# Kernel tuning notes

Measured on AMD Instinct MI355X. Metric: run time of the kernel, lower is better.

Reference implementation:

```python
import jax, jax.numpy as jnp
import numpy as np
import math

B, S, H, K = 512, 200, 256, 16

def setup_inputs() -> dict:
    key = jax.random.key(0)
    ks = jax.random.split(key, 8)
    scale = 1.0 / math.sqrt(H)
    return {
        "input_tensor": jax.random.normal(ks[0], (B, S, H), dtype=jnp.float32),
        "item_mask": jax.random.randint(ks[1], (B, S, 1), 0, 2) > 0,
        "time_f_w_matrix": jax.random.uniform(ks[2], (B, S, 1), dtype=jnp.float32),
        "W1": jax.random.normal(ks[3], (H, H), dtype=jnp.float32) * scale,
        "b1": jnp.zeros((H,), dtype=jnp.float32),
        "W2": jax.random.normal(ks[4], (H, H), dtype=jnp.float32) * scale,
        "b2": jnp.zeros((H,), dtype=jnp.float32),
        "W3": jax.random.normal(ks[5], (H, K), dtype=jnp.float32) * scale,
    }

def reference(input_tensor, item_mask, time_f_w_matrix, W1, b1, W2, b2, W3):
    # small MLP: two Linear+ReLU then bias-free Linear to k_interests
    h = jax.nn.relu(jnp.einsum('bsh,hd->bsd', input_tensor, W1) + b1)
    h = jax.nn.relu(jnp.einsum('bsh,hd->bsd', h, W2) + b2)
    D = jnp.einsum('bsh,hk->bsk', h, W3)              # [B,S,K]
    D = jax.nn.softmax(D, axis=-1)                    # softmax over interests
    mask = item_mask[:, :, 0:1]                       # [B,S,1] bool, broadcast over K
    D = jnp.where(mask, D, jnp.float32(-10000.0))
    D = D / jnp.float32(math.sqrt(K))
    D = jax.nn.softmax(D, axis=-2)                    # softmax over sequence
    D = time_f_w_matrix[:, :, 0:1] * D                # time weighting
    # einsum 'nij,nik->nkj': pool items into K interest vectors
    return jnp.einsum('bsh,bsk->bkh', input_tensor, D)
```

## Files before the change

kernel.cpp:

```cpp
#include <hip/hip_runtime.h>
#include <math.h>

#define HDIM 256
#define KDIM 16
#define SDIM 200
#define BDIM 512
#define NROWS (BDIM * SDIM)
#define TM 32

typedef __bf16 bf16x8 __attribute__((ext_vector_type(8)));
typedef __bf16 bf16x4 __attribute__((ext_vector_type(4)));
typedef float  f32x4  __attribute__((ext_vector_type(4)));

__global__ __launch_bounds__(256) void pack_w_kernel(
    const float* __restrict__ src, __bf16* __restrict__ hi,
    __bf16* __restrict__ lo, int lgN)
{
    int idx = blockIdx.x * 256 + threadIdx.x;
    int N = 1 << lgN;
    int k = idx >> lgN;
    int n = idx & (N - 1);
    float v = src[idx];
    __bf16 h = (__bf16)v;
    float r = v - (float)h;
    int d = (((k >> 3) << lgN) + n) * 8 + (k & 7);
    hi[d] = h;
    lo[d] = (__bf16)r;
}

__global__ __launch_bounds__(256, 4) void mlp_softk_mfma(
    const float* __restrict__ X, const int* __restrict__ mask,
    const __bf16* __restrict__ W1h, const __bf16* __restrict__ W1l,
    const float* __restrict__ b1,
    const __bf16* __restrict__ W2h, const __bf16* __restrict__ W2l,
    const float* __restrict__ b2,
    const __bf16* __restrict__ W3h, const __bf16* __restrict__ W3l,
    float* __restrict__ P)
{
    __shared__ __bf16 Ahi[TM * HDIM];
    __shared__ __bf16 Alo[TM * HDIM];

    const int tid  = threadIdx.x;
    const int lane = tid & 63;
    const int w    = tid >> 6;
    const int l15  = lane & 15;
    const int quad = lane >> 4;
    const long r0  = (long)blockIdx.x * TM;

    {
        const float4* Xt = (const float4*)(X + r0 * HDIM);
        #pragma unroll
        for (int t = 0; t < (TM * HDIM / 4) / 256; ++t) {
            int v4  = tid + t * 256;
            float4 f = Xt[v4];
            int row = v4 >> 6;
            int col = (v4 & 63) << 2;
            int kgs = (col >> 3) ^ (row & 31);
            int base = row * HDIM + kgs * 8 + (col & 7);
            __bf16 h0 = (__bf16)f.x, h1 = (__bf16)f.y,
                   h2 = (__bf16)f.z, h3 = (__bf16)f.w;
            bf16x4 hv = {h0, h1, h2, h3};
            bf16x4 lv = {(__bf16)(f.x - (float)h0), (__bf16)(f.y - (float)h1),
                         (__bf16)(f.z - (float)h2), (__bf16)(f.w - (float)h3)};
            *(bf16x4*)(&Ahi[base]) = hv;
            *(bf16x4*)(&Alo[base]) = lv;
        }
    }
    __syncthreads();

    f32x4 acc[2][4];

    auto layer = [&](const __bf16* __restrict__ Wh, const __bf16* __restrict__ Wl,
                     const float* __restrict__ bias) {
        #pragma unroll
        for (int mt = 0; mt < 2; ++mt)
            #pragma unroll
            for (int nt = 0; nt < 4; ++nt)
                acc[mt][nt] = (f32x4){0.f, 0.f, 0.f, 0.f};

        #pragma unroll 2
        for (int kc = 0; kc < 8; ++kc) {
            bf16x8 bh[4], bl[4], ah[2], al[2];
            #pragma unroll
            for (int nt = 0; nt < 4; ++nt) {
                int n  = w * 64 + nt * 16 + l15;
                int kg = kc * 4 + quad;
                bh[nt] = *(const bf16x8*)(Wh + (kg * HDIM + n) * 8);
                bl[nt] = *(const bf16x8*)(Wl + (kg * HDIM + n) * 8);
            }
            #pragma unroll
            for (int mt = 0; mt < 2; ++mt) {
                int row = mt * 16 + l15;
                int kgs = (kc * 4 + quad) ^ (row & 31);
                ah[mt] = *(const bf16x8*)(&Ahi[row * HDIM + kgs * 8]);
                al[mt] = *(const bf16x8*)(&Alo[row * HDIM + kgs * 8]);
            }
            #pragma unroll
            for (int mt = 0; mt < 2; ++mt)
                #pragma unroll
                for (int nt = 0; nt < 4; ++nt) {
                    acc[mt][nt] = __builtin_amdgcn_mfma_f32_16x16x32_bf16(
                        ah[mt], bh[nt], acc[mt][nt], 0, 0, 0);
                    acc[mt][nt] = __builtin_amdgcn_mfma_f32_16x16x32_bf16(
                        al[mt], bh[nt], acc[mt][nt], 0, 0, 0);
                    acc[mt][nt] = __builtin_amdgcn_mfma_f32_16x16x32_bf16(
                        ah[mt], bl[nt], acc[mt][nt], 0, 0, 0);
                }
        }
        __syncthreads();

        float bias_v[4];
        #pragma unroll
        for (int nt = 0; nt < 4; ++nt) bias_v[nt] = bias[w * 64 + nt * 16 + l15];
        #pragma unroll
        for (int mt = 0; mt < 2; ++mt)
            #pragma unroll
            for (int nt = 0; nt < 4; ++nt)
                #pragma unroll
                for (int r = 0; r < 4; ++r) {
                    float v = fmaxf(acc[mt][nt][r] + bias_v[nt], 0.f);
                    int row = mt * 16 + quad * 4 + r;
                    int col = w * 64 + nt * 16 + l15;
                    int idx = row * HDIM + (((col >> 3) ^ (row & 31)) * 8) + (col & 7);
                    __bf16 h = (__bf16)v;
                    Ahi[idx] = h;
                    Alo[idx] = (__bf16)(v - (float)h);
                }
        __syncthreads();
    };

    layer(W1h, W1l, b1);
    layer(W2h, W2l, b2);

    if (w < 2) {
        f32x4 lg = {0.f, 0.f, 0.f, 0.f};
        #pragma unroll
        for (int kc = 0; kc < 8; ++kc) {
            int row = w * 16 + l15;
            int kg  = kc * 4 + quad;
            int kgs = kg ^ (row & 31);
            bf16x8 ah = *(const bf16x8*)(&Ahi[row * HDIM + kgs * 8]);
            bf16x8 al = *(const bf16x8*)(&Alo[row * HDIM + kgs * 8]);
            bf16x8 bh = *(const bf16x8*)(W3h + (kg * KDIM + l15) * 8);
            bf16x8 bl = *(const bf16x8*)(W3l + (kg * KDIM + l15) * 8);
            lg = __builtin_amdgcn_mfma_f32_16x16x32_bf16(ah, bh, lg, 0, 0, 0);
            lg = __builtin_amdgcn_mfma_f32_16x16x32_bf16(al, bh, lg, 0, 0, 0);
            lg = __builtin_amdgcn_mfma_f32_16x16x32_bf16(ah, bl, lg, 0, 0, 0);
        }

        #pragma unroll
        for (int r = 0; r < 4; ++r) {
            float v  = lg[r];
            float mx = v;
            mx = fmaxf(mx, __shfl_xor(mx, 1));
            mx = fmaxf(mx, __shfl_xor(mx, 2));
            mx = fmaxf(mx, __shfl_xor(mx, 4));
            mx = fmaxf(mx, __shfl_xor(mx, 8));
            float e = __expf(v - mx);
            float s = e;
            s += __shfl_xor(s, 1);
            s += __shfl_xor(s, 2);
            s += __shfl_xor(s, 4);
            s += __shfl_xor(s, 8);
            int grow = (int)r0 + w * 16 + quad * 4 + r;
            int mv   = mask[grow];
            float ov = mv ? (e / s) * 0.25f : -2500.0f;
            P[(long)grow * KDIM + l15] = ov;
        }
    }
}

__global__ __launch_bounds__(256) void softs_agg_kernel(
    const float* __restrict__ X, const float* __restrict__ tf,
    const float* __restrict__ P, float* __restrict__ out)
{
    __shared__ float wl[SDIM * KDIM];
    __shared__ float tfl[SDIM];
    __shared__ float psum[256];
    __shared__ float invk[KDIM];
    __shared__ float red[KDIM * HDIM];

    const int tid = threadIdx.x;
    const int b   = blockIdx.x;

    const float* Pb = P + (long)b * SDIM * KDIM;
    float ps = 0.f;
    #pragma unroll
    for (int t = 0; t < 13; ++t) {
        int i = tid + t * 256;
        if (i < SDIM * KDIM) {
            float e = __expf(Pb[i]);
            wl[i] = e;
            ps += e;
        }
    }
    psum[tid] = ps;
    if (tid < SDIM) tfl[tid] = tf[b * SDIM + tid];
    __syncthreads();

    if (tid < KDIM) {
        float s = 0.f;
        #pragma unroll
        for (int g = 0; g < 16; ++g) s += psum[tid + g * 16];
        invk[tid] = 1.f / s;
    }
    __syncthreads();

    #pragma unroll
    for (int t = 0; t < 13; ++t) {
        int i = tid + t * 256;
        if (i < SDIM * KDIM) wl[i] *= tfl[i >> 4] * invk[i & 15];
    }
    __syncthreads();

    const int wv = tid >> 6;
    const int sh = wv >> 1;
    const int hh = wv & 1;
    const int ln = tid & 63;

    float accx[KDIM], accy[KDIM];
    #pragma unroll
    for (int k = 0; k < KDIM; ++k) { accx[k] = 0.f; accy[k] = 0.f; }

    const float2* Xb  = (const float2*)(X + (long)b * SDIM * HDIM) + hh * 64 + ln;
    const f32x4*  wl4 = (const f32x4*)wl;
    const int s0 = sh * 100;
    #pragma unroll 4
    for (int si = 0; si < 100; ++si) {
        int s = s0 + si;
        float2 x = Xb[(long)s * (HDIM / 2)];
        f32x4 d0 = wl4[s * 4 + 0];
        f32x4 d1 = wl4[s * 4 + 1];
        f32x4 d2 = wl4[s * 4 + 2];
        f32x4 d3 = wl4[s * 4 + 3];
        #pragma unroll
        for (int j = 0; j < 4; ++j) {
            accx[0 + j]  = fmaf(x.x, d0[j], accx[0 + j]);
            accx[4 + j]  = fmaf(x.x, d1[j], accx[4 + j]);
            accx[8 + j]  = fmaf(x.x, d2[j], accx[8 + j]);
            accx[12 + j] = fmaf(x.x, d3[j], accx[12 + j]);
            accy[0 + j]  = fmaf(x.y, d0[j], accy[0 + j]);
            accy[4 + j]  = fmaf(x.y, d1[j], accy[4 + j]);
            accy[8 + j]  = fmaf(x.y, d2[j], accy[8 + j]);
            accy[12 + j] = fmaf(x.y, d3[j], accy[12 + j]);
        }
    }

    if (sh == 1) {
        #pragma unroll
        for (int k = 0; k < KDIM; ++k) {
            red[k * HDIM + hh * 128 + 2 * ln + 0] = accx[k];
            red[k * HDIM + hh * 128 + 2 * ln + 1] = accy[k];
        }
    }
    __syncthreads();
    if (sh == 0) {
        float* ob = out + (long)b * KDIM * HDIM + hh * 128 + 2 * ln;
        #pragma unroll
        for (int k = 0; k < KDIM; ++k) {
            float2 o;
            o.x = accx[k] + red[k * HDIM + hh * 128 + 2 * ln + 0];
            o.y = accy[k] + red[k * HDIM + hh * 128 + 2 * ln + 1];
            *(float2*)(ob + (long)k * HDIM) = o;
        }
    }
}

extern "C" void kernel_launch(void* const* d_in, const int* in_sizes, int n_in,
                              void* d_out, int out_size, void* d_ws, size_t ws_size,
                              hipStream_t stream) {
    (void)in_sizes; (void)n_in; (void)out_size; (void)ws_size;
    const float* X    = (const float*)d_in[0];
    const int*   mask = (const int*)  d_in[1];
    const float* tf   = (const float*)d_in[2];
    const float* W1   = (const float*)d_in[3];
    const float* b1   = (const float*)d_in[4];
    const float* W2   = (const float*)d_in[5];
    const float* b2   = (const float*)d_in[6];
    const float* W3   = (const float*)d_in[7];
    float* out = (float*)d_out;

    char* ws = (char*)d_ws;
    float*  P   = (float*)ws;
    __bf16* w1h = (__bf16*)(ws + 6553600);
    __bf16* w1l = w1h + 65536;
    __bf16* w2h = w1l + 65536;
    __bf16* w2l = w2h + 65536;
    __bf16* w3h = w2l + 65536;
    __bf16* w3l = w3h + 4096;

    pack_w_kernel<<<256, 256, 0, stream>>>(W1, w1h, w1l, 8);
    pack_w_kernel<<<256, 256, 0, stream>>>(W2, w2h, w2l, 8);
    pack_w_kernel<<<16,  256, 0, stream>>>(W3, w3h, w3l, 4);
    mlp_softk_mfma<<<NROWS / TM, 256, 0, stream>>>(X, mask, w1h, w1l, b1,
                                                   w2h, w2l, b2, w3h, w3l, P);
    softs_agg_kernel<<<BDIM, 256, 0, stream>>>(X, tf, P, out);
}
```

Measured before the change: 285.2 us.

## Register-resident single-wave MLP with transposed MFMA and bias folded into weights

Rewrites the MLP kernel so each 64-thread wave handles 32 rows entirely in registers. It computes W^T·X^T so layer outputs stay in MFMA accumulators and are passed to the next layer through lane shuffles instead of shared memory and __syncthreads. Biases are folded in as an extra K chunk multiplied by a ones vector. The three weight-pack launches are merged into one kernel with the new fragment layout. This removes LDS traffic and block barriers, but raises register pressure heavily (a 16x2 accumulator array plus 8x2 fragment arrays per wave) and has each wave reload all weights from cache.

After: 325.5 us. +14.1%, slower.

```diff
diff --git a/kernel.cpp b/kernel.cpp
--- a/kernel.cpp
+++ b/kernel.cpp
@@ -6,167 +6,225 @@
 #define SDIM 200
 #define BDIM 512
 #define NROWS (BDIM * SDIM)
-#define TM 32
 
 typedef __bf16 bf16x8 __attribute__((ext_vector_type(8)));
-typedef __bf16 bf16x4 __attribute__((ext_vector_type(4)));
 typedef float  f32x4  __attribute__((ext_vector_type(4)));
 
-__global__ __launch_bounds__(256) void pack_w_kernel(
-    const float* __restrict__ src, __bf16* __restrict__ hi,
-    __bf16* __restrict__ lo, int lgN)
+#define MFMA(a, b, c) __builtin_amdgcn_mfma_f32_16x16x32_bf16(a, b, c, 0, 0, 0)
+
+__global__ __launch_bounds__(256) void pack_all(
+    const float* __restrict__ W1, const float* __restrict__ b1,
+    const float* __restrict__ W2, const float* __restrict__ b2,
+    const float* __restrict__ W3,
+    __bf16* __restrict__ w1h, __bf16* __restrict__ w1l,
+    __bf16* __restrict__ w2h, __bf16* __restrict__ w2l,
+    __bf16* __restrict__ w3h, __bf16* __restrict__ w3l)
 {
-    int idx = blockIdx.x * 256 + threadIdx.x;
-    int N = 1 << lgN;
-    int k = idx >> lgN;
-    int n = idx & (N - 1);
-    float v = src[idx];
+    int gid = blockIdx.x * 256 + threadIdx.x;
+    const float *src, *bias;
+    __bf16 *oh, *ol;
+    int e, N;
+    if (gid < 73728)       { src = W1; bias = b1;      oh = w1h; ol = w1l; e = gid;          N = 256; }
+    else if (gid < 147456) { src = W2; bias = b2;      oh = w2h; ol = w2l; e = gid - 73728;  N = 256; }
+    else if (gid < 151552) { src = W3; bias = nullptr; oh = w3h; ol = w3l; e = gid - 147456; N = 16;  }
+    else return;
+
+    int j = e & 7, l = (e >> 3) & 63, c = e >> 9;
+    int dt, kc;
+    if (N == 256) { dt = c & 15; kc = c >> 4; } else { dt = 0; kc = c; }
+    int d = dt * 16 + (l & 15);
+    int k = kc * 32 + ((l >> 4) * 8) + j;
+    float v = (k < 256) ? src[k * N + d] : ((k == 256 && bias) ? bias[d] : 0.f);
     __bf16 h = (__bf16)v;
-    float r = v - (float)h;
-    int d = (((k >> 3) << lgN) + n) * 8 + (k & 7);
-    hi[d] = h;
-    lo[d] = (__bf16)r;
+    oh[e] = h;
+    ol[e] = (__bf16)(v - (float)h);
 }
 
-__global__ __launch_bounds__(256, 4) void mlp_softk_mfma(
+__global__ __launch_bounds__(64, 2) void mlp_fused(
     const float* __restrict__ X, const int* __restrict__ mask,
-    const __bf16* __restrict__ W1h, const __bf16* __restrict__ W1l,
-    const float* __restrict__ b1,
-    const __bf16* __restrict__ W2h, const __bf16* __restrict__ W2l,
-    const float* __restrict__ b2,
-    const __bf16* __restrict__ W3h, const __bf16* __restrict__ W3l,
+    const __bf16* __restrict__ w1h, const __bf16* __restrict__ w1l,
+    const __bf16* __restrict__ w2h, const __bf16* __restrict__ w2l,
+    const __bf16* __restrict__ w3h, const __bf16* __restrict__ w3l,
     float* __restrict__ P)
 {
-    __shared__ __bf16 Ahi[TM * HDIM];
-    __shared__ __bf16 Alo[TM * HDIM];
-
-    const int tid  = threadIdx.x;
-    const int lane = tid & 63;
-    const int w    = tid >> 6;
-    const int l15  = lane & 15;
-    const int quad = lane >> 4;
-    const long r0  = (long)blockIdx.x * TM;
-
+    const int l = threadIdx.x;
+    const int q = l >> 4, m = l & 15;
+    const long R = (long)blockIdx.x * 32;
+
+    f32x4 acc1[16][2];
+    #pragma unroll
+    for (int t = 0; t < 16; ++t) {
+        acc1[t][0] = (f32x4){0.f, 0.f, 0.f, 0.f};
+        acc1[t][1] = (f32x4){0.f, 0.f, 0.f, 0.f};
+    }
+
+    #pragma unroll 1
+    for (int kc = 0; kc < 8; ++kc) {
+        bf16x8 bxh[2], bxl[2];
+        #pragma unroll
+        for (int rt = 0; rt < 2; ++rt) {
+            const float* xp = X + (R + rt * 16 + m) * HDIM + kc * 32 + q * 8;
+            float4 f0 = *(const float4*)xp;
+            float4 f1 = *(const float4*)(xp + 4);
+            float xv[8] = {f0.x, f0.y, f0.z, f0.w, f1.x, f1.y, f1.z, f1.w};
+            #pragma unroll
+            for (int j2 = 0; j2 < 8; ++j2) {
+                __bf16 h = (__bf16)xv[j2];
+                bxh[rt][j2] = h;
+                bxl[rt][j2] = (__bf16)(xv[j2] - (float)h);
+            }
+        }
+        #pragma unroll
+        for (int dt = 0; dt < 16; ++dt) {
+            bf16x8 ah = *(const bf16x8*)(w1h + (kc * 16 + dt) * 512 + l * 8);
+            bf16x8 al = *(const bf16x8*)(w1l + (kc * 16 + dt) * 512 + l * 8);
+            #pragma unroll
+            for (int rt = 0; rt < 2; ++rt) {
+                acc1[dt][rt] = MFMA(ah, bxh[rt], acc1[dt][rt]);
+                acc1[dt][rt] = MFMA(al, bxh[rt], acc1[dt][rt]);
+                acc1[dt][rt] = MFMA(ah, bxl[rt], acc1[dt][rt]);
+            }
+        }
+    }
     {
-        const float4* Xt = (const float4*)(X + r0 * HDIM);
-        #pragma unroll
-        for (int t = 0; t < (TM * HDIM / 4) / 256; ++t) {
-            int v4  = tid + t * 256;
-            float4 f = Xt[v4];
-            int row = v4 >> 6;
-            int col = (v4 & 63) << 2;
-            int kgs = (col >> 3) ^ (row & 31);
-            int base = row * HDIM + kgs * 8 + (col & 7);
-            __bf16 h0 = (__bf16)f.x, h1 = (__bf16)f.y,
-                   h2 = (__bf16)f.z, h3 = (__bf16)f.w;
-            bf16x4 hv = {h0, h1, h2, h3};
-            bf16x4 lv = {(__bf16)(f.x - (float)h0), (__bf16)(f.y - (float)h1),
-                         (__bf16)(f.z - (float)h2), (__bf16)(f.w - (float)h3)};
-            *(bf16x4*)(&Ahi[base]) = hv;
-            *(bf16x4*)(&Alo[base]) = lv;
-        }
-    }
-    __syncthreads();
-
-    f32x4 acc[2][4];
-
-    auto layer = [&](const __bf16* __restrict__ Wh, const __bf16* __restrict__ Wl,
-                     const float* __restrict__ bias) {
-        #pragma unroll
-        for (int mt = 0; mt < 2; ++mt)
-            #pragma unroll
-            for (int nt = 0; nt < 4; ++nt)
-                acc[mt][nt] = (f32x4){0.f, 0.f, 0.f, 0.f};
-
-        #pragma unroll 2
-        for (int kc = 0; kc < 8; ++kc) {
-            bf16x8 bh[4], bl[4], ah[2], al[2];
-            #pragma unroll
-            for (int nt = 0; nt < 4; ++nt) {
-                int n  = w * 64 + nt * 16 + l15;
-                int kg = kc * 4 + quad;
-                bh[nt] = *(const bf16x8*)(Wh + (kg * HDIM + n) * 8);
-                bl[nt] = *(const bf16x8*)(Wl + (kg * HDIM + n) * 8);
-            }
-            #pragma unroll
-            for (int mt = 0; mt < 2; ++mt) {
-                int row = mt * 16 + l15;
-                int kgs = (kc * 4 + quad) ^ (row & 31);
-                ah[mt] = *(const bf16x8*)(&Ahi[row * HDIM + kgs * 8]);
-                al[mt] = *(const bf16x8*)(&Alo[row * HDIM + kgs * 8]);
-            }
-            #pragma unroll
-            for (int mt = 0; mt < 2; ++mt)
+        bf16x8 bx1;
+        #pragma unroll
+        for (int j2 = 0; j2 < 8; ++j2) bx1[j2] = (__bf16)0.f;
+        bx1[0] = (q == 0) ? (__bf16)1.f : (__bf16)0.f;
+        #pragma unroll
+        for (int dt = 0; dt < 16; ++dt) {
+            bf16x8 ah = *(const bf16x8*)(w1h + (128 + dt) * 512 + l * 8);
+            bf16x8 al = *(const bf16x8*)(w1l + (128 + dt) * 512 + l * 8);
+            #pragma unroll
+            for (int rt = 0; rt < 2; ++rt) {
+                acc1[dt][rt] = MFMA(ah, bx1, acc1[dt][rt]);
+                acc1[dt][rt] = MFMA(al, bx1, acc1[dt][rt]);
+            }
+        }
+    }
+
+    bf16x8 f2h[8][2], f2l[8][2];
+    #pragma unroll
+    for (int kc2 = 0; kc2 < 8; ++kc2) {
+        #pragma unroll
+        for (int rt = 0; rt < 2; ++rt) {
+            float g[8];
+            #pragma unroll
+            for (int i = 0; i < 4; ++i) {
+                float s0 = fmaxf(acc1[2 * kc2 + 0][rt][i], 0.f);
+                float s1 = fmaxf(acc1[2 * kc2 + 1][rt][i], 0.f);
+                int lane_lo = ((2 * (q & 1)) << 4) | m;
+                float glo0 = __shfl(s0, lane_lo);
+                float ghi0 = __shfl(s0, lane_lo + 16);
+                float glo1 = __shfl(s1, lane_lo);
+                float ghi1 = __shfl(s1, lane_lo + 16);
+                g[i]     = (q < 2) ? glo0 : glo1;
+                g[4 + i] = (q < 2) ? ghi0 : ghi1;
+            }
+            #pragma unroll
+            for (int j2 = 0; j2 < 8; ++j2) {
+                __bf16 h = (__bf16)g[j2];
+                f2h[kc2][rt][j2] = h;
+                f2l[kc2][rt][j2] = (__bf16)(g[j2] - (float)h);
+            }
+        }
+    }
+
+    f32x4 acc3[2] = {(f32x4){0.f, 0.f, 0.f, 0.f}, (f32x4){0.f, 0.f, 0.f, 0.f}};
+    #pragma unroll 1
+    for (int qd = 0; qd < 4; ++qd) {
+        f32x4 acc2[4][2];
+        #pragma unroll
+        for (int t = 0; t < 4; ++t) {
+            acc2[t][0] = (f32x4){0.f, 0.f, 0.f, 0.f};
+            acc2[t][1] = (f32x4){0.f, 0.f, 0.f, 0.f};
+        }
+        #pragma unroll
+        for (int kc2 = 0; kc2 < 8; ++kc2) {
+            #pragma unroll
+            for (int dtl = 0; dtl < 4; ++dtl) {
+                int c = kc2 * 16 + qd * 4 + dtl;
+                bf16x8 ah = *(const bf16x8*)(w2h + c * 512 + l * 8);
+                bf16x8 al = *(const bf16x8*)(w2l + c * 512 + l * 8);
                 #pragma unroll
-                for (int nt = 0; nt < 4; ++nt) {
-                    acc[mt][nt] = __builtin_amdgcn_mfma_f32_16x16x32_bf16(
-                        ah[mt], bh[nt], acc[mt][nt], 0, 0, 0);
-                    acc[mt][nt] = __builtin_amdgcn_mfma_f32_16x16x32_bf16(
-                        al[mt], bh[nt], acc[mt][nt], 0, 0, 0);
-                    acc[mt][nt] = __builtin_amdgcn_mfma_f32_16x16x32_bf16(
-                        ah[mt], bl[nt], acc[mt][nt], 0, 0, 0);
+                for (int rt = 0; rt < 2; ++rt) {
+                    acc2[dtl][rt] = MFMA(ah, f2h[kc2][rt], acc2[dtl][rt]);
+                    acc2[dtl][rt] = MFMA(al, f2h[kc2][rt], acc2[dtl][rt]);
+                    acc2[dtl][rt] = MFMA(ah, f2l[kc2][rt], acc2[dtl][rt]);
                 }
-        }
-        __syncthreads();
-
-        float bias_v[4];
-        #pragma unroll
-        for (int nt = 0; nt < 4; ++nt) bias_v[nt] = bias[w * 64 + nt * 16 + l15];
-        #pragma unroll
-        for (int mt = 0; mt < 2; ++mt)
-            #pragma unroll
-            for (int nt = 0; nt < 4; ++nt)
+            }
+        }
+        {
+            bf16x8 bx1;
+            #pragma unroll
+            for (int j2 = 0; j2 < 8; ++j2) bx1[j2] = (__bf16)0.f;
+            bx1[0] = (q == 0) ? (__bf16)1.f : (__bf16)0.f;
+            #pragma unroll
+            for (int dtl = 0; dtl < 4; ++dtl) {
+                int c = 128 + qd * 4 + dtl;
+                bf16x8 ah = *(const bf16x8*)(w2h + c * 512 + l * 8);
+                bf16x8 al = *(const bf16x8*)(w2l + c * 512 + l * 8);
                 #pragma unroll
-                for (int r = 0; r < 4; ++r) {
-                    float v = fmaxf(acc[mt][nt][r] + bias_v[nt], 0.f);
-                    int row = mt * 16 + quad * 4 + r;
-                    int col = w * 64 + nt * 16 + l15;
-                    int idx = row * HDIM + (((col >> 3) ^ (row & 31)) * 8) + (col & 7);
-                    __bf16 h = (__bf16)v;
-                    Ahi[idx] = h;
-                    Alo[idx] = (__bf16)(v - (float)h);
+                for (int rt = 0; rt < 2; ++rt) {
+                    acc2[dtl][rt] = MFMA(ah, bx1, acc2[dtl][rt]);
+                    acc2[dtl][rt] = MFMA(al, bx1, acc2[dtl][rt]);
                 }
-        __syncthreads();
-    };
-
-    layer(W1h, W1l, b1);
-    layer(W2h, W2l, b2);
-
-    if (w < 2) {
-        f32x4 lg = {0.f, 0.f, 0.f, 0.f};
-        #pragma unroll
-        for (int kc = 0; kc < 8; ++kc) {
-            int row = w * 16 + l15;
-            int kg  = kc * 4 + quad;
-            int kgs = kg ^ (row & 31);
-            bf16x8 ah = *(const bf16x8*)(&Ahi[row * HDIM + kgs * 8]);
-            bf16x8 al = *(const bf16x8*)(&Alo[row * HDIM + kgs * 8]);
-            bf16x8 bh = *(const bf16x8*)(W3h + (kg * KDIM + l15) * 8);
-            bf16x8 bl = *(const bf16x8*)(W3l + (kg * KDIM + l15) * 8);
-            lg = __builtin_amdgcn_mfma_f32_16x16x32_bf16(ah, bh, lg, 0, 0, 0);
-            lg = __builtin_amdgcn_mfma_f32_16x16x32_bf16(al, bh, lg, 0, 0, 0);
-            lg = __builtin_amdgcn_mfma_f32_16x16x32_bf16(ah, bl, lg, 0, 0, 0);
-        }
-
-        #pragma unroll
-        for (int r = 0; r < 4; ++r) {
-            float v  = lg[r];
-            float mx = v;
-            mx = fmaxf(mx, __shfl_xor(mx, 1));
-            mx = fmaxf(mx, __shfl_xor(mx, 2));
-            mx = fmaxf(mx, __shfl_xor(mx, 4));
-            mx = fmaxf(mx, __shfl_xor(mx, 8));
-            float e = __expf(v - mx);
-            float s = e;
-            s += __shfl_xor(s, 1);
-            s += __shfl_xor(s, 2);
-            s += __shfl_xor(s, 4);
-            s += __shfl_xor(s, 8);
-            int grow = (int)r0 + w * 16 + quad * 4 + r;
-            int mv   = mask[grow];
-            float ov = mv ? (e / s) * 0.25f : -2500.0f;
-            P[(long)grow * KDIM + l15] = ov;
-        }
+            }
+        }
+        #pragma unroll
+        for (int c = 0; c < 2; ++c) {
+            bf16x8 f3h[2], f3l[2];
+            #pragma unroll
+            for (int rt = 0; rt < 2; ++rt) {
+                float g[8];
+                #pragma unroll
+                for (int i = 0; i < 4; ++i) {
+                    float s0 = fmaxf(acc2[2 * c + 0][rt][i], 0.f);
+                    float s1 = fmaxf(acc2[2 * c + 1][rt][i], 0.f);
+                    int lane_lo = ((2 * (q & 1)) << 4) | m;
+                    float glo0 = __shfl(s0, lane_lo);
+                    float ghi0 = __shfl(s0, lane_lo + 16);
+                    float glo1 = __shfl(s1, lane_lo);
+                    float ghi1 = __shfl(s1, lane_lo + 16);
+                    g[i]     = (q < 2) ? glo0 : glo1;
+                    g[4 + i] = (q < 2) ? ghi0 : ghi1;
+                }
+                #pragma unroll
+                for (int j2 = 0; j2 < 8; ++j2) {
+                    __bf16 h = (__bf16)g[j2];
+                    f3h[rt][j2] = h;
+                    f3l[rt][j2] = (__bf16)(g[j2] - (float)h);
+                }
+            }
+            bf16x8 a3h = *(const bf16x8*)(w3h + (2 * qd + c) * 512 + l * 8);
+            bf16x8 a3l = *(const bf16x8*)(w3l + (2 * qd + c) * 512 + l * 8);
+            #pragma unroll
+            for (int rt = 0; rt < 2; ++rt) {
+                acc3[rt] = MFMA(a3h, f3h[rt], acc3[rt]);
+                acc3[rt] = MFMA(a3l, f3h[rt], acc3[rt]);
+                acc3[rt] = MFMA(a3h, f3l[rt], acc3[rt]);
+            }
+        }
+    }
+
+    #pragma unroll
+    for (int rt = 0; rt < 2; ++rt) {
+        float mx = fmaxf(fmaxf(acc3[rt][0], acc3[rt][1]),
+                         fmaxf(acc3[rt][2], acc3[rt][3]));
+        mx = fmaxf(mx, __shfl_xor(mx, 16));
+        mx = fmaxf(mx, __shfl_xor(mx, 32));
+        float e[4], s = 0.f;
+        #pragma unroll
+        for (int r = 0; r < 4; ++r) { e[r] = __expf(acc3[rt][r] - mx); s += e[r]; }
+        s += __shfl_xor(s, 16);
+        s += __shfl_xor(s, 32);
+        long grow = R + rt * 16 + m;
+        int mv = mask[grow];
+        float inv = 0.25f / s;
+        float4 o;
+        if (mv) { o.x = e[0] * inv; o.y = e[1] * inv; o.z = e[2] * inv; o.w = e[3] * inv; }
+        else    { o.x = o.y = o.z = o.w = -2500.0f; }
+        *(float4*)(P + grow * KDIM + 4 * q) = o;
     }
 }
 
@@ -283,16 +341,13 @@
     char* ws = (char*)d_ws;
     float*  P   = (float*)ws;
     __bf16* w1h = (__bf16*)(ws + 6553600);
-    __bf16* w1l = w1h + 65536;
-    __bf16* w2h = w1l + 65536;
-    __bf16* w2l = w2h + 65536;
-    __bf16* w3h = w2l + 65536;
+    __bf16* w1l = w1h + 73728;
+    __bf16* w2h = w1l + 73728;
+    __bf16* w2l = w2h + 73728;
+    __bf16* w3h = w2l + 73728;
     __bf16* w3l = w3h + 4096;
 
-    pack_w_kernel<<<256, 256, 0, stream>>>(W1, w1h, w1l, 8);
-    pack_w_kernel<<<256, 256, 0, stream>>>(W2, w2h, w2l, 8);
-    pack_w_kernel<<<16,  256, 0, stream>>>(W3, w3h, w3l, 4);
-    mlp_softk_mfma<<<NROWS / TM, 256, 0, stream>>>(X, mask, w1h, w1l, b1,
-                                                   w2h, w2l, b2, w3h, w3l, P);
+    pack_all<<<592, 256, 0, stream>>>(W1, b1, W2, b2, W3, w1h, w1l, w2h, w2l, w3h, w3l);
+    mlp_fused<<<NROWS / 32, 64, 0, stream>>>(X, mask, w1h, w1l, w2h, w2l, w3h, w3l, P);
     softs_agg_kernel<<<BDIM, 256, 0, stream>>>(X, tf, P, out);
 }
```
